# Optimization experiments

Measured on AMD Instinct MI355X. Metric: run time of the kernel, lower is better.

The kernel has to match this reference:

```python
import jax, jax.numpy as jnp
import numpy as np

B, L, F, A, H = 512, 196, 512, 512, 512  # batch, att locations, feature, att hidden, rnn hidden


def setup_inputs() -> dict:
    key = jax.random.key(0)
    ks = jax.random.split(key, 12)
    s = 0.02
    return {
        "xt": jax.random.normal(ks[0], (B, H), jnp.float32),
        "fc_feats": jax.random.normal(ks[1], (B, F), jnp.float32),
        "att_feats": jax.random.normal(ks[2], (B, L, F), jnp.float32),
        "h0": jax.random.normal(ks[3], (1, B, H), jnp.float32),
        "c0": jax.random.normal(ks[4], (1, B, H), jnp.float32),
        "W_ctx": jax.random.normal(ks[5], (A, F), jnp.float32) * s,
        "b_ctx": jnp.zeros((A,), jnp.float32),
        "W_hid": jax.random.normal(ks[6], (A, H), jnp.float32) * s,
        "b_hid": jnp.zeros((A,), jnp.float32),
        "w_score": jax.random.normal(ks[7], (A,), jnp.float32) * s,
        "b_score": jnp.zeros((), jnp.float32),
        "W_ih": jax.random.normal(ks[8], (4 * H, H + F), jnp.float32) * s,
        "W_hh": jax.random.normal(ks[9], (4 * H, H), jnp.float32) * s,
    }


def reference(xt, fc_feats, att_feats, h0, c0, W_ctx, b_ctx, W_hid, b_hid,
              w_score, b_score, W_ih, W_hh):
    h_prev = h0[-1]  # (B, H)
    c_prev = c0[-1]  # (B, H)
    # Bahdanau additive attention
    img_att = jnp.einsum('blf,af->bla', att_feats, W_ctx) + b_ctx          # (B, L, A)
    hid_att = h_prev @ W_hid.T + b_hid                                     # (B, A)
    alignment = jnp.tanh(img_att + hid_att[:, None, :])                    # (B, L, A)
    scores = jnp.einsum('bla,a->bl', alignment, w_score) + b_score         # (B, L)
    score = jax.nn.softmax(scores, axis=-1)                                # (B, L)
    att_res = jnp.einsum('bl,blf->bf', score, att_feats)                   # (B, F)
    # Single LSTM step, PyTorch gate order (i, f, g, o), no bias
    x = jnp.concatenate([xt, att_res], axis=1)                             # (B, H+F)
    gates = x @ W_ih.T + h_prev @ W_hh.T                                   # (B, 4H)
    i, f, g, o = jnp.split(gates, 4, axis=1)
    i = jax.nn.sigmoid(i)
    f = jax.nn.sigmoid(f)
    g = jnp.tanh(g)
    o = jax.nn.sigmoid(o)
    c = f * c_prev + i * g
    h = o * jnp.tanh(c)
    return h, (h[None], c[None])
```

## Files before the change

kernel.cpp:

```cpp
#include <hip/hip_runtime.h>
#include <stdint.h>

typedef unsigned short u16;
typedef unsigned int   u32;
typedef __attribute__((ext_vector_type(2))) float f32x2;
typedef __attribute__((ext_vector_type(4))) float f32x4;
typedef __attribute__((ext_vector_type(8))) short s16x8;

__device__ __forceinline__ u16 f2bf(float f) {
    u32 x = __float_as_uint(f);
    x += 0x7fffu + ((x >> 16) & 1u);
    return (u16)(x >> 16);
}
__device__ __forceinline__ float tanh_fast(float x) {
    return 1.f - 2.f / (__expf(2.f * x) + 1.f);
}
__device__ __forceinline__ float sigm(float x) {
    return 1.f / (1.f + __expf(-x));
}

#define BM 128
#define BN 128
#define BK 64

__device__ __forceinline__ s16x8 cvt8(const float* p) {
    union { s16x8 v; u32 w[4]; } r;
    f32x4 x0 = *(const f32x4*)p;
    f32x4 x1 = *(const f32x4*)(p + 4);
    r.w[0] = __builtin_amdgcn_perm(__float_as_uint(x0[1]), __float_as_uint(x0[0]), 0x07060302u);
    r.w[1] = __builtin_amdgcn_perm(__float_as_uint(x0[3]), __float_as_uint(x0[2]), 0x07060302u);
    r.w[2] = __builtin_amdgcn_perm(__float_as_uint(x1[1]), __float_as_uint(x1[0]), 0x07060302u);
    r.w[3] = __builtin_amdgcn_perm(__float_as_uint(x1[3]), __float_as_uint(x1[2]), 0x07060302u);
    return r.v;
}

template<int EPI, bool AF32, bool BF32>
__global__ __launch_bounds__(256) void gemm_bt(
    const void* __restrict__ Ag, const void* __restrict__ B1, const void* __restrict__ B2,
    int lda, int ldb1, int ldb2, int ksplitB, int N, int klen,
    float* __restrict__ outF,
    const float* __restrict__ bias1, const float* __restrict__ bias2,
    const float* __restrict__ hidb, const float* __restrict__ wscore,
    float* __restrict__ scores)
{
    __shared__ __align__(16) u16 As[BM * BK];
    __shared__ __align__(16) u16 Bs[BN * BK];
    const int tid = threadIdx.x;
    const int l   = tid & 63;
    const int m0  = blockIdx.y * BM;
    const int n0  = blockIdx.x * BN;
    const int kbeg = blockIdx.z * klen;
    const int kend = kbeg + klen;
    const int w  = tid >> 6;
    const int wr = (w >> 1) * 64;
    const int wc = (w & 1) * 64;
    const int srow = tid >> 3;
    const int skc  = (tid & 7) * 8;

    f32x4 acc[4][4] = {};

    for (int kt = kbeg; kt < kend; kt += BK) {
        s16x8 va[4], vb[4];
        #pragma unroll
        for (int c = 0; c < 4; ++c) {
            int row = c * 32 + srow;
            size_t aoff = (size_t)(m0 + row) * lda + kt + skc;
            if constexpr (AF32) va[c] = cvt8((const float*)Ag + aoff);
            else                va[c] = *(const s16x8*)((const u16*)Ag + aoff);
            int kg = kt + skc;
            if constexpr (BF32) {
                const float* bp = (kg < ksplitB)
                    ? ((const float*)B1 + (size_t)(n0 + row) * ldb1 + kg)
                    : ((const float*)B2 + (size_t)(n0 + row) * ldb2 + (kg - ksplitB));
                vb[c] = cvt8(bp);
            } else {
                const u16* bp = (kg < ksplitB)
                    ? ((const u16*)B1 + (size_t)(n0 + row) * ldb1 + kg)
                    : ((const u16*)B2 + (size_t)(n0 + row) * ldb2 + (kg - ksplitB));
                vb[c] = *(const s16x8*)bp;
            }
        }
        __syncthreads();
        #pragma unroll
        for (int c = 0; c < 4; ++c) {
            int row = c * 32 + srow;
            *(s16x8*)(As + row * BK + skc) = va[c];
            *(s16x8*)(Bs + row * BK + skc) = vb[c];
        }
        __syncthreads();
        #pragma unroll
        for (int kk = 0; kk < BK; kk += 32) {
            s16x8 af[4], bg[4];
            #pragma unroll
            for (int i = 0; i < 4; ++i)
                af[i] = *(const s16x8*)(As + (wr + i * 16 + (l & 15)) * BK + kk + (l >> 4) * 8);
            #pragma unroll
            for (int j = 0; j < 4; ++j)
                bg[j] = *(const s16x8*)(Bs + (wc + j * 16 + (l & 15)) * BK + kk + (l >> 4) * 8);
            #pragma unroll
            for (int i = 0; i < 4; ++i)
                #pragma unroll
                for (int j = 0; j < 4; ++j)
                    acc[i][j] = __builtin_amdgcn_mfma_f32_16x16x32_bf16(af[i], bg[j], acc[i][j], 0, 0, 0);
        }
    }

    const int col0 = l & 15;
    const int rgrp = l >> 4;

    if (EPI == 0) {
        #pragma unroll
        for (int j = 0; j < 4; ++j) {
            int gcol = n0 + wc + j * 16 + col0;
            float bsum = bias1[gcol] + bias2[gcol];
            #pragma unroll
            for (int i = 0; i < 4; ++i)
                #pragma unroll
                for (int q = 0; q < 4; ++q) {
                    int grow = m0 + wr + i * 16 + rgrp * 4 + q;
                    outF[(size_t)grow * N + gcol] = acc[i][j][q] + bsum;
                }
        }
    } else if (EPI == 1) {
        float wsv[4]; int gcol[4];
        #pragma unroll
        for (int j = 0; j < 4; ++j) {
            gcol[j] = n0 + wc + j * 16 + col0;
            wsv[j] = wscore[gcol[j]];
        }
        #pragma unroll
        for (int i = 0; i < 4; ++i) {
            #pragma unroll
            for (int q = 0; q < 4; ++q) {
                int grow = m0 + wr + i * 16 + rgrp * 4 + q;
                int bb = grow / 196;
                const float* hb = hidb + (size_t)bb * N;
                float s = 0.f;
                #pragma unroll
                for (int j = 0; j < 4; ++j) {
                    float x = acc[i][j][q] + hb[gcol[j]];
                    s += tanh_fast(x) * wsv[j];
                }
                s += __shfl_xor(s, 1);
                s += __shfl_xor(s, 2);
                s += __shfl_xor(s, 4);
                s += __shfl_xor(s, 8);
                if (col0 == 0) atomicAdd(&scores[grow], s);
            }
        }
    } else {
        #pragma unroll
        for (int j = 0; j < 4; ++j) {
            int gcol = n0 + wc + j * 16 + col0;
            #pragma unroll
            for (int i = 0; i < 4; ++i)
                #pragma unroll
                for (int q = 0; q < 4; ++q) {
                    int grow = m0 + wr + i * 16 + rgrp * 4 + q;
                    atomicAdd(&outF[(size_t)grow * N + gcol], acc[i][j][q]);
                }
        }
    }
}

__global__ __launch_bounds__(256) void softmax_attres(
    const float* __restrict__ att, const float* __restrict__ scores,
    const float* __restrict__ xt, const float* __restrict__ h0,
    u16* __restrict__ X)
{
    const int b = blockIdx.x;
    const int tid = threadIdx.x;
    __shared__ float p[200];
    __shared__ float redm[4], reds[4];

    float s = (tid < 196) ? scores[b * 196 + tid] : -3.0e38f;
    float m = s;
    #pragma unroll
    for (int d = 32; d; d >>= 1) m = fmaxf(m, __shfl_xor(m, d));
    if ((tid & 63) == 0) redm[tid >> 6] = m;
    __syncthreads();
    m = fmaxf(fmaxf(redm[0], redm[1]), fmaxf(redm[2], redm[3]));

    float e = (tid < 196) ? __expf(s - m) : 0.f;
    float sum = e;
    #pragma unroll
    for (int d = 32; d; d >>= 1) sum += __shfl_xor(sum, d);
    if ((tid & 63) == 0) reds[tid >> 6] = sum;
    __syncthreads();
    sum = reds[0] + reds[1] + reds[2] + reds[3];
    if (tid < 196) p[tid] = e / sum;
    __syncthreads();

    const f32x2* att2 = (const f32x2*)(att + (size_t)b * 196 * 512);
    float a0 = 0.f, a1 = 0.f;
    for (int lq = 0; lq < 196; ++lq) {
        f32x2 u = att2[(size_t)lq * 256 + tid];
        float pl = p[lq];
        a0 = fmaf(pl, u[0], a0);
        a1 = fmaf(pl, u[1], a1);
    }
    u16* Xr = X + (size_t)b * 1536;
    ((u32*)(Xr + 512))[tid] = ((u32)f2bf(a1) << 16) | (u32)f2bf(a0);
    f32x2 xv = ((const f32x2*)(xt + (size_t)b * 512))[tid];
    ((u32*)Xr)[tid] = ((u32)f2bf(xv[1]) << 16) | (u32)f2bf(xv[0]);
    f32x2 hv = ((const f32x2*)(h0 + (size_t)b * 512))[tid];
    ((u32*)(Xr + 1024))[tid] = ((u32)f2bf(hv[1]) << 16) | (u32)f2bf(hv[0]);
}

__global__ __launch_bounds__(256) void lstm_ep(
    const float* __restrict__ gates, const float* __restrict__ c0, float* __restrict__ out)
{
    int idx = blockIdx.x * 256 + threadIdx.x;
    int b = idx >> 9, hh = idx & 511;
    const float* g = gates + ((size_t)b << 11);
    float i_ = sigm(g[hh]);
    float f_ = sigm(g[512 + hh]);
    float g_ = tanh_fast(g[1024 + hh]);
    float o_ = sigm(g[1536 + hh]);
    float c = f_ * c0[idx] + i_ * g_;
    float h = o_ * tanh_fast(c);
    out[idx] = h;
    out[262144 + idx] = h;
    out[524288 + idx] = c;
}

extern "C" void kernel_launch(void* const* d_in, const int* in_sizes, int n_in,
                              void* d_out, int out_size, void* d_ws, size_t ws_size,
                              hipStream_t stream) {
    const float* xt   = (const float*)d_in[0];
    const float* att  = (const float*)d_in[2];
    const float* h0   = (const float*)d_in[3];
    const float* c0   = (const float*)d_in[4];
    const float* Wctx = (const float*)d_in[5];
    const float* bctx = (const float*)d_in[6];
    const float* Whid = (const float*)d_in[7];
    const float* bhid = (const float*)d_in[8];
    const float* wsc  = (const float*)d_in[9];
    const float* Wih  = (const float*)d_in[11];
    const float* Whh  = (const float*)d_in[12];
    float* out = (float*)d_out;

    char* ws = (char*)d_ws;
    float* hidb   = (float*)(ws);
    float* scores = (float*)(ws + 1048576);
    float* gates  = (float*)(ws + 1449984);
    u16*   X      = (u16*)  (ws + 5644288);

    hipMemsetAsync(ws + 1048576, 0, 4595712, stream);

    gemm_bt<0, true, true><<<dim3(4, 4, 1), 256, 0, stream>>>(
        h0, Whid, Whid, 512, 512, 512, 1 << 28, 512, 512,
        hidb, bhid, bctx, nullptr, nullptr, nullptr);

    gemm_bt<1, true, true><<<dim3(4, 784, 1), 256, 0, stream>>>(
        att, Wctx, Wctx, 512, 512, 512, 1 << 28, 512, 512,
        nullptr, nullptr, nullptr, hidb, wsc, scores);

    softmax_attres<<<512, 256, 0, stream>>>(att, scores, xt, h0, X);

    gemm_bt<2, false, true><<<dim3(16, 4, 4), 256, 0, stream>>>(
        X, Wih, Whh, 1536, 1024, 512, 1024, 2048, 384,
        gates, nullptr, nullptr, nullptr, nullptr, nullptr);

    lstm_ep<<<1024, 256, 0, stream>>>(gates, c0, out);
}
```

Measured before the change: 521.0 us.

## Prefetch GEMM tiles, swizzle LDS, remap workgroups, split-K hid GEMM, widen attres loads

```diff
diff --git a/kernel.cpp b/kernel.cpp
--- a/kernel.cpp
+++ b/kernel.cpp
@@ -18,21 +18,18 @@
 __device__ __forceinline__ float sigm(float x) {
     return 1.f / (1.f + __expf(-x));
 }
-
-#define BM 128
-#define BN 128
-#define BK 64
-
-__device__ __forceinline__ s16x8 cvt8(const float* p) {
+__device__ __forceinline__ s16x8 pack8(f32x4 x0, f32x4 x1) {
     union { s16x8 v; u32 w[4]; } r;
-    f32x4 x0 = *(const f32x4*)p;
-    f32x4 x1 = *(const f32x4*)(p + 4);
     r.w[0] = __builtin_amdgcn_perm(__float_as_uint(x0[1]), __float_as_uint(x0[0]), 0x07060302u);
     r.w[1] = __builtin_amdgcn_perm(__float_as_uint(x0[3]), __float_as_uint(x0[2]), 0x07060302u);
     r.w[2] = __builtin_amdgcn_perm(__float_as_uint(x1[1]), __float_as_uint(x1[0]), 0x07060302u);
     r.w[3] = __builtin_amdgcn_perm(__float_as_uint(x1[3]), __float_as_uint(x1[2]), 0x07060302u);
     return r.v;
 }
+
+#define BM 128
+#define BN 128
+#define BK 64
 
 template<int EPI, bool AF32, bool BF32>
 __global__ __launch_bounds__(256) void gemm_bt(
@@ -47,56 +44,84 @@
     __shared__ __align__(16) u16 Bs[BN * BK];
     const int tid = threadIdx.x;
     const int l   = tid & 63;
-    const int m0  = blockIdx.y * BM;
-    const int n0  = blockIdx.x * BN;
-    const int kbeg = blockIdx.z * klen;
-    const int kend = kbeg + klen;
+
+    const int nbx = gridDim.x;
+    const int nwg = nbx * gridDim.y;
+    const int p   = blockIdx.x + blockIdx.y * nbx;
+    const int per = nwg >> 3;
+    const int lg  = (p & 7) * per + (p >> 3);
+    const int n0  = (lg % nbx) * BN;
+    const int m0  = (lg / nbx) * BM;
+
+    const int kbeg   = blockIdx.z * klen;
+    const int nsteps = klen / BK;
     const int w  = tid >> 6;
     const int wr = (w >> 1) * 64;
     const int wc = (w & 1) * 64;
     const int srow = tid >> 3;
-    const int skc  = (tid & 7) * 8;
+    const int cs   = tid & 7;
 
     f32x4 acc[4][4] = {};
-
-    for (int kt = kbeg; kt < kend; kt += BK) {
-        s16x8 va[4], vb[4];
+    f32x4 fa[8], fb[8];
+    s16x8 ha[4], hb16[4];
+
+    auto LOAD = [&](int kt) {
         #pragma unroll
         for (int c = 0; c < 4; ++c) {
             int row = c * 32 + srow;
-            size_t aoff = (size_t)(m0 + row) * lda + kt + skc;
-            if constexpr (AF32) va[c] = cvt8((const float*)Ag + aoff);
-            else                va[c] = *(const s16x8*)((const u16*)Ag + aoff);
-            int kg = kt + skc;
+            if constexpr (AF32) {
+                const float* ap = (const float*)Ag + (size_t)(m0 + row) * lda + kt + cs * 8;
+                fa[2*c]   = *(const f32x4*)ap;
+                fa[2*c+1] = *(const f32x4*)(ap + 4);
+            } else {
+                ha[c] = *(const s16x8*)((const u16*)Ag + (size_t)(m0 + row) * lda + kt + cs * 8);
+            }
+            int kg = kt + cs * 8;
             if constexpr (BF32) {
                 const float* bp = (kg < ksplitB)
                     ? ((const float*)B1 + (size_t)(n0 + row) * ldb1 + kg)
                     : ((const float*)B2 + (size_t)(n0 + row) * ldb2 + (kg - ksplitB));
-                vb[c] = cvt8(bp);
+                fb[2*c]   = *(const f32x4*)bp;
+                fb[2*c+1] = *(const f32x4*)(bp + 4);
             } else {
                 const u16* bp = (kg < ksplitB)
                     ? ((const u16*)B1 + (size_t)(n0 + row) * ldb1 + kg)
                     : ((const u16*)B2 + (size_t)(n0 + row) * ldb2 + (kg - ksplitB));
-                vb[c] = *(const s16x8*)bp;
-            }
-        }
+                hb16[c] = *(const s16x8*)bp;
+            }
+        }
+    };
+
+    LOAD(kbeg);
+
+    for (int s = 0; s < nsteps; ++s) {
         __syncthreads();
         #pragma unroll
         for (int c = 0; c < 4; ++c) {
             int row = c * 32 + srow;
-            *(s16x8*)(As + row * BK + skc) = va[c];
-            *(s16x8*)(Bs + row * BK + skc) = vb[c];
+            int sw = ((cs ^ (row & 7)) * 8);
+            s16x8 va, vb;
+            if constexpr (AF32) va = pack8(fa[2*c], fa[2*c+1]); else va = ha[c];
+            if constexpr (BF32) vb = pack8(fb[2*c], fb[2*c+1]); else vb = hb16[c];
+            *(s16x8*)(As + row * BK + sw) = va;
+            *(s16x8*)(Bs + row * BK + sw) = vb;
         }
         __syncthreads();
+        if (s + 1 < nsteps) LOAD(kbeg + (s + 1) * BK);
         #pragma unroll
         for (int kk = 0; kk < BK; kk += 32) {
             s16x8 af[4], bg[4];
-            #pragma unroll
-            for (int i = 0; i < 4; ++i)
-                af[i] = *(const s16x8*)(As + (wr + i * 16 + (l & 15)) * BK + kk + (l >> 4) * 8);
-            #pragma unroll
-            for (int j = 0; j < 4; ++j)
-                bg[j] = *(const s16x8*)(Bs + (wc + j * 16 + (l & 15)) * BK + kk + (l >> 4) * 8);
+            const int cb = (kk >> 3) + (l >> 4);
+            #pragma unroll
+            for (int i = 0; i < 4; ++i) {
+                int ra = wr + i * 16 + (l & 15);
+                af[i] = *(const s16x8*)(As + ra * BK + ((cb ^ (ra & 7)) * 8));
+            }
+            #pragma unroll
+            for (int j = 0; j < 4; ++j) {
+                int rb = wc + j * 16 + (l & 15);
+                bg[j] = *(const s16x8*)(Bs + rb * BK + ((cb ^ (rb & 7)) * 8));
+            }
             #pragma unroll
             for (int i = 0; i < 4; ++i)
                 #pragma unroll
@@ -108,25 +133,13 @@
     const int col0 = l & 15;
     const int rgrp = l >> 4;
 
-    if (EPI == 0) {
-        #pragma unroll
-        for (int j = 0; j < 4; ++j) {
-            int gcol = n0 + wc + j * 16 + col0;
-            float bsum = bias1[gcol] + bias2[gcol];
-            #pragma unroll
-            for (int i = 0; i < 4; ++i)
-                #pragma unroll
-                for (int q = 0; q < 4; ++q) {
-                    int grow = m0 + wr + i * 16 + rgrp * 4 + q;
-                    outF[(size_t)grow * N + gcol] = acc[i][j][q] + bsum;
-                }
-        }
-    } else if (EPI == 1) {
-        float wsv[4]; int gcol[4];
+    if (EPI == 1) {
+        float wsv[4], bs[4]; int gcol[4];
         #pragma unroll
         for (int j = 0; j < 4; ++j) {
             gcol[j] = n0 + wc + j * 16 + col0;
             wsv[j] = wscore[gcol[j]];
+            bs[j]  = bias1[gcol[j]] + bias2[gcol[j]];
         }
         #pragma unroll
         for (int i = 0; i < 4; ++i) {
@@ -138,7 +151,7 @@
                 float s = 0.f;
                 #pragma unroll
                 for (int j = 0; j < 4; ++j) {
-                    float x = acc[i][j][q] + hb[gcol[j]];
+                    float x = acc[i][j][q] + hb[gcol[j]] + bs[j];
                     s += tanh_fast(x) * wsv[j];
                 }
                 s += __shfl_xor(s, 1);
@@ -172,6 +185,7 @@
     const int tid = threadIdx.x;
     __shared__ float p[200];
     __shared__ float redm[4], reds[4];
+    __shared__ float accu[128 * 4];
 
     float s = (tid < 196) ? scores[b * 196 + tid] : -3.0e38f;
     float m = s;
@@ -191,16 +205,28 @@
     if (tid < 196) p[tid] = e / sum;
     __syncthreads();
 
-    const f32x2* att2 = (const f32x2*)(att + (size_t)b * 196 * 512);
-    float a0 = 0.f, a1 = 0.f;
-    for (int lq = 0; lq < 196; ++lq) {
-        f32x2 u = att2[(size_t)lq * 256 + tid];
+    const float* attb = att + (size_t)b * 196 * 512;
+    const int half = tid >> 7;
+    const int e4   = (tid & 127) * 4;
+    f32x4 a = {0.f, 0.f, 0.f, 0.f};
+    for (int lq = half; lq < 196; lq += 2) {
+        f32x4 u = *(const f32x4*)(attb + (size_t)lq * 512 + e4);
         float pl = p[lq];
-        a0 = fmaf(pl, u[0], a0);
-        a1 = fmaf(pl, u[1], a1);
-    }
+        a[0] = fmaf(pl, u[0], a[0]);
+        a[1] = fmaf(pl, u[1], a[1]);
+        a[2] = fmaf(pl, u[2], a[2]);
+        a[3] = fmaf(pl, u[3], a[3]);
+    }
+    if (half) *(f32x4*)(accu + (tid & 127) * 4) = a;
+    __syncthreads();
+
     u16* Xr = X + (size_t)b * 1536;
-    ((u32*)(Xr + 512))[tid] = ((u32)f2bf(a1) << 16) | (u32)f2bf(a0);
+    if (!half) {
+        f32x4 o = *(const f32x4*)(accu + tid * 4);
+        a[0] += o[0]; a[1] += o[1]; a[2] += o[2]; a[3] += o[3];
+        ((u32*)(Xr + 512))[tid * 2]     = ((u32)f2bf(a[1]) << 16) | (u32)f2bf(a[0]);
+        ((u32*)(Xr + 512))[tid * 2 + 1] = ((u32)f2bf(a[3]) << 16) | (u32)f2bf(a[2]);
+    }
     f32x2 xv = ((const f32x2*)(xt + (size_t)b * 512))[tid];
     ((u32*)Xr)[tid] = ((u32)f2bf(xv[1]) << 16) | (u32)f2bf(xv[0]);
     f32x2 hv = ((const f32x2*)(h0 + (size_t)b * 512))[tid];
@@ -246,15 +272,15 @@
     float* gates  = (float*)(ws + 1449984);
     u16*   X      = (u16*)  (ws + 5644288);
 
-    hipMemsetAsync(ws + 1048576, 0, 4595712, stream);
-
-    gemm_bt<0, true, true><<<dim3(4, 4, 1), 256, 0, stream>>>(
-        h0, Whid, Whid, 512, 512, 512, 1 << 28, 512, 512,
-        hidb, bhid, bctx, nullptr, nullptr, nullptr);
+    hipMemsetAsync(ws, 0, 5644288, stream);
+
+    gemm_bt<2, true, true><<<dim3(4, 4, 4), 256, 0, stream>>>(
+        h0, Whid, Whid, 512, 512, 512, 1 << 28, 512, 128,
+        hidb, nullptr, nullptr, nullptr, nullptr, nullptr);
 
     gemm_bt<1, true, true><<<dim3(4, 784, 1), 256, 0, stream>>>(
         att, Wctx, Wctx, 512, 512, 512, 1 << 28, 512, 512,
-        nullptr, nullptr, nullptr, hidb, wsc, scores);
+        nullptr, bhid, bctx, hidb, wsc, scores);
 
     softmax_attres<<<512, 256, 0, stream>>>(att, scores, xt, h0, X);
 
```

New measurement: 511.5 us. Within noise of the previous version (-1.8%).
